# Optimization experiments

Measured on AMD Instinct MI355X. Metric: run time of the kernel, lower is better.

The kernel has to match this reference:

```python
import jax, jax.numpy as jnp
import numpy as np

N = 100000      # nodes
E = 1600000     # edges
F_IN = 256      # nfeat
F_OUT = 128     # out channels


def setup_inputs() -> dict:
    key = jax.random.key(0)
    k1, k2, k3 = jax.random.split(key, 3)
    feature = jax.random.normal(k1, (N, F_IN), dtype=jnp.float32)
    edge_index = jax.random.randint(k2, (2, E), 0, N, dtype=jnp.int32)
    # glorot-ish init for the GCN linear weight
    W = jax.random.normal(k3, (F_IN, F_OUT), dtype=jnp.float32) * (1.0 / np.sqrt(F_IN))
    b = jnp.zeros((F_OUT,), dtype=jnp.float32)
    return {"feature": feature, "edge_index": edge_index, "W": W, "b": b}


def reference(feature, edge_index, W, b):
    # GCNConv (PyG defaults): add self-loops, symmetric normalization,
    # linear transform then scatter-add aggregation to destination nodes.
    x = feature @ W                                   # [N, F_OUT]
    loops = jnp.arange(N, dtype=edge_index.dtype)
    row = jnp.concatenate([edge_index[0], loops])     # source nodes [E+N]
    col = jnp.concatenate([edge_index[1], loops])     # dest   nodes [E+N]
    ones = jnp.ones(row.shape[0], dtype=x.dtype)
    deg = jax.ops.segment_sum(ones, col, num_segments=N)   # in-degree incl. self-loop
    dinv = jnp.where(deg > 0, jax.lax.rsqrt(deg), 0.0)     # deg^{-1/2}
    norm = dinv[row] * dinv[col]                            # [E+N]
    msg = x[row] * norm[:, None]                            # gather + scale
    agg = jax.ops.segment_sum(msg, col, num_segments=N)     # scatter-add
    x_out = jax.nn.relu(agg + b)                            # [N, F_OUT]
    h = jax.nn.sigmoid(jnp.mean(x_out, axis=0))             # [F_OUT]
    return (x_out, h)
```

## Files before the change

### kernel.cpp

```cpp
#include <hip/hip_runtime.h>
#include <hip/hip_bf16.h>

typedef __attribute__((ext_vector_type(8))) short short8;
typedef __attribute__((ext_vector_type(4))) float floatx4;
typedef unsigned short u16;
typedef unsigned int u32;
typedef unsigned long long u64;

#define F_IN  256
#define F_OUT 128
#define CAP   64
#define NWIN  8
#define PRE   24

__device__ __forceinline__ float bf_lo(u32 u) { return __uint_as_float(u << 16); }
__device__ __forceinline__ float bf_hi(u32 u) { return __uint_as_float(u & 0xffff0000u); }
__device__ __forceinline__ u16 f2bf(float f) {
    u32 u = __float_as_uint(f);
    u += 0x7fffu + ((u >> 16) & 1u);
    return (u16)(u >> 16);
}

__global__ void k_pack(const float* __restrict__ W, u16* __restrict__ Wp,
                       u16* __restrict__ xw, int N) {
    int gid = blockIdx.x * 256 + threadIdx.x;
    if (gid < 32768) {
        int f = gid >> 3, j = gid & 7;
        int lane = f & 63, tt = (f >> 6) & 7, kb = f >> 9;
        int m = lane & 15, q = lane >> 4;
        Wp[(size_t)f * 8 + j] = f2bf(W[(kb * 32 + q * 8 + j) * F_OUT + tt * 16 + m]);
    } else {
        int e = gid - 32768;
        if (e < 128) {
            int w = e >> 4, m = e & 15;
            xw[((size_t)w * (N + 1) + N) * 16 + m] = 0;
        }
    }
}

__global__ void k_fillcap_xcd(const int* __restrict__ rowi, const int* __restrict__ coli,
                              int E, int npw, int N,
                              int* __restrict__ cursor, int* __restrict__ csr) {
    int grp  = blockIdx.x & (NWIN - 1);
    int gblk = blockIdx.x >> 3;
    int nblk = gridDim.x >> 3;
    int lo = grp * npw;
    int hi = lo + npw; if (hi > N) hi = N;
    for (int e = gblk * blockDim.x + threadIdx.x; e < E; e += nblk * blockDim.x) {
        int d = coli[e];
        if (d >= lo && d < hi) {
            int r = rowi[e];
            int p = atomicAdd(&cursor[d], 1);
            if (p < CAP) csr[((size_t)d << 6) + p] = r;
        }
    }
}

__global__ void k_degree(const int* __restrict__ col, int E, int* __restrict__ deg) {
    for (int e = blockIdx.x * blockDim.x + threadIdx.x; e < E; e += gridDim.x * blockDim.x)
        atomicAdd(&deg[col[e]], 1);
}

__global__ void k_blocksum(const int* __restrict__ deg, int N, int* __restrict__ bsum) {
    __shared__ int s[256];
    int base = blockIdx.x * 1024, t = threadIdx.x;
    int v = 0;
    for (int i = t; i < 1024; i += 256) { int idx = base + i; v += (idx < N) ? deg[idx] : 0; }
    s[t] = v; __syncthreads();
    for (int off = 128; off > 0; off >>= 1) {
        if (t < off) s[t] += s[t + off];
        __syncthreads();
    }
    if (t == 0) bsum[blockIdx.x] = s[0];
}

__global__ void k_rowptr(const int* __restrict__ deg, int N, const int* __restrict__ bsum,
                         int nb, int* __restrict__ rowptr) {
    __shared__ int s[256];
    __shared__ int sb[256];
    int base = blockIdx.x * 1024, t = threadIdx.x;
    sb[t] = (t < nb && t < blockIdx.x) ? bsum[t] : 0;
    __syncthreads();
    for (int off = 128; off > 0; off >>= 1) {
        if (t < off) sb[t] += sb[t + off];
        __syncthreads();
    }
    int blockbase = sb[0];
    int v[4]; int tot = 0;
#pragma unroll
    for (int j = 0; j < 4; ++j) {
        int idx = base + t * 4 + j;
        v[j] = (idx < N) ? deg[idx] : 0;
        tot += v[j];
    }
    s[t] = tot; __syncthreads();
    for (int off = 1; off < 256; off <<= 1) {
        int x = (t >= off) ? s[t - off] : 0;
        __syncthreads();
        s[t] += x;
        __syncthreads();
    }
    int prefix = blockbase + s[t] - tot;
#pragma unroll
    for (int j = 0; j < 4; ++j) {
        int idx = base + t * 4 + j;
        if (idx < N) rowptr[idx] = prefix;
        prefix += v[j];
    }
}

__global__ void k_fill(const int* __restrict__ rowi, const int* __restrict__ coli, int E,
                       const int* __restrict__ rowptr, int* __restrict__ cursor,
                       int* __restrict__ csr) {
    for (int e = blockIdx.x * blockDim.x + threadIdx.x; e < E; e += gridDim.x * blockDim.x) {
        int d = coli[e];
        int p = atomicAdd(&cursor[d], 1);
        csr[rowptr[d] + p] = rowi[e];
    }
}

__global__ __launch_bounds__(256) void k_gemm(
        const float* __restrict__ feat, const int* __restrict__ deg,
        const u16* __restrict__ Wp, u16* __restrict__ xw, int N) {
    __shared__ u16 atile[64 * 264];
    const int t = threadIdx.x, wave = t >> 6, lane = t & 63;
    const int m = lane & 15, q = lane >> 4;
    const int base = blockIdx.x * 64;

    for (int r = wave; r < 64; r += 4) {
        int i = base + r;
        float ax = 0.f, ay = 0.f, az = 0.f, aw = 0.f;
        if (i < N) {
            float di = rsqrtf((float)(deg[i] + 1));
            float4 v = *(const float4*)(feat + (size_t)i * F_IN + lane * 4);
            ax = di * v.x; ay = di * v.y; az = di * v.z; aw = di * v.w;
        }
        u32* dst = (u32*)(atile + r * 264 + lane * 4);
        dst[0] = ((u32)f2bf(ay) << 16) | (u32)f2bf(ax);
        dst[1] = ((u32)f2bf(aw) << 16) | (u32)f2bf(az);
    }
    __syncthreads();

    floatx4 acc[8];
#pragma unroll
    for (int tt = 0; tt < 8; ++tt) acc[tt] = (floatx4)0.0f;
    const short8* wp = (const short8*)Wp;
#pragma unroll
    for (int kb = 0; kb < 8; ++kb) {
        short8 a0 = *(const short8*)(atile + (wave * 16 + m) * 264 + kb * 32 + q * 8);
#pragma unroll
        for (int tt = 0; tt < 8; ++tt) {
            short8 b = wp[(kb * 8 + tt) * 64 + lane];
            acc[tt] = __builtin_amdgcn_mfma_f32_16x16x32_bf16(a0, b, acc[tt], 0, 0, 0);
        }
    }

#pragma unroll
    for (int r = 0; r < 4; ++r) {
        int orow = base + wave * 16 + q * 4 + r;
        if (orow < N) {
#pragma unroll
            for (int tt = 0; tt < 8; ++tt)
                xw[((size_t)tt * (N + 1) + orow) * 16 + m] = f2bf(acc[tt][r]);
        }
    }
}

__global__ __launch_bounds__(256) void k_agg(const u16* __restrict__ xw,
                                             const int* __restrict__ rowptr,
                                             const int* __restrict__ deg,
                                             const int* __restrict__ csr,
                                             const float* __restrict__ bvec,
                                             float* __restrict__ out,
                                             float* __restrict__ hsum, int N) {
    __shared__ float hpart[16];
    int t = threadIdx.x;
    if (t < 16) hpart[t] = 0.f;
    __syncthreads();
    const int w = blockIdx.x & 7;
    const int stripe = blockIdx.x >> 3;
    const int nstripe = gridDim.x >> 3;
    const int lane = t & 63, wv = t >> 6;
    const int lane3 = lane & 3;
    const int g = lane >> 2;
    const int gbase = lane & 60;
    const u32* slice = (const u32*)xw + (size_t)w * (N + 1) * 8;
    const float4 bv = *(const float4*)(bvec + w * 16 + lane3 * 4);
    float h0 = 0.f, h1 = 0.f, h2 = 0.f, h3 = 0.f;
    const int step = nstripe * 64;
    for (int i = stripe * 64 + wv * 16 + g; i < N; i += step) {
        int dd = deg[i];
        float di = rsqrtf((float)(dd + 1));
        int s0;
        if (rowptr) s0 = rowptr[i];
        else { s0 = i << 6; dd = dd < CAP ? dd : CAP; }
        u64 xs = *(const u64*)(slice + (u32)(i * 8) + lane3 * 2);
        u32 xsl = (u32)xs, xsh = (u32)(xs >> 32);
        float a0 = bf_lo(xsl), a1 = bf_hi(xsl), a2 = bf_lo(xsh), a3 = bf_hi(xsh);
        int s[6];
#pragma unroll
        for (int c = 0; c < 6; ++c) s[c] = csr[s0 + c * 4 + lane3];
#pragma unroll
        for (int c = 0; c < 6; ++c) s[c] = (c * 4 + lane3 < dd) ? s[c] : N;
        u64 xv[PRE];
#pragma unroll
        for (int u = 0; u < PRE; ++u) {
            int sx = __shfl(s[u >> 2], gbase + (u & 3));
            xv[u] = *(const u64*)(slice + (u32)(sx * 8) + lane3 * 2);
        }
#pragma unroll
        for (int u = 0; u < PRE; ++u) {
            u32 lo = (u32)xv[u], hi = (u32)(xv[u] >> 32);
            a0 += bf_lo(lo); a1 += bf_hi(lo); a2 += bf_lo(hi); a3 += bf_hi(hi);
        }
        if (__any(dd > PRE)) {
            int ddmax = dd;
            ddmax = max(ddmax, __shfl_xor(ddmax, 4));
            ddmax = max(ddmax, __shfl_xor(ddmax, 8));
            ddmax = max(ddmax, __shfl_xor(ddmax, 16));
            ddmax = max(ddmax, __shfl_xor(ddmax, 32));
            ddmax = min(ddmax, rowptr ? (1 << 20) : CAP);
            for (int jb = PRE; jb < ddmax; jb += 4) {
                int sxv = N;
                if (jb + lane3 < dd) sxv = csr[s0 + jb + lane3];
                u64 yv[4];
#pragma unroll
                for (int u = 0; u < 4; ++u) {
                    int sx = __shfl(sxv, gbase + u);
                    yv[u] = *(const u64*)(slice + (u32)(sx * 8) + lane3 * 2);
                }
#pragma unroll
                for (int u = 0; u < 4; ++u) {
                    u32 lo = (u32)yv[u], hi = (u32)(yv[u] >> 32);
                    a0 += bf_lo(lo); a1 += bf_hi(lo); a2 += bf_lo(hi); a3 += bf_hi(hi);
                }
            }
        }
        float o0 = fmaxf(fmaf(a0, di, bv.x), 0.f);
        float o1 = fmaxf(fmaf(a1, di, bv.y), 0.f);
        float o2 = fmaxf(fmaf(a2, di, bv.z), 0.f);
        float o3 = fmaxf(fmaf(a3, di, bv.w), 0.f);
        h0 += o0; h1 += o1; h2 += o2; h3 += o3;
        *(float4*)(out + (size_t)i * F_OUT + w * 16 + lane3 * 4) =
            make_float4(o0, o1, o2, o3);
    }
    atomicAdd(&hpart[lane3 * 4 + 0], h0);
    atomicAdd(&hpart[lane3 * 4 + 1], h1);
    atomicAdd(&hpart[lane3 * 4 + 2], h2);
    atomicAdd(&hpart[lane3 * 4 + 3], h3);
    __syncthreads();
    if (t < 16) atomicAdd(&hsum[w * 16 + t], hpart[t]);
}

__global__ void k_h(const float* __restrict__ hsum, float* __restrict__ outh, float invN) {
    int t = threadIdx.x;
    if (t < 128) {
        float mm = hsum[t] * invN;
        outh[t] = 1.f / (1.f + __expf(-mm));
    }
}

extern "C" void kernel_launch(void* const* d_in, const int* in_sizes, int n_in,
                              void* d_out, int out_size, void* d_ws, size_t ws_size,
                              hipStream_t stream) {
    const float* feat = (const float*)d_in[0];
    const int* ei     = (const int*)d_in[1];
    const float* W    = (const float*)d_in[2];
    const float* bvec = (const float*)d_in[3];
    float* out        = (float*)d_out;

    const int N = in_sizes[0] / F_IN;
    const int E = in_sizes[1] / 2;

    char* ws = (char*)d_ws;
    size_t o = 0;
    u16* Wp       = (u16*)(ws + o);   o += (size_t)F_IN * F_OUT * 2;
    int* deg      = (int*)(ws + o);   o += (size_t)N * 4;
    int* cursor   = (int*)(ws + o);   o += (size_t)N * 4;
    float* hsum   = (float*)(ws + o); o += 512;
    int* rowptr   = (int*)(ws + o);   o += (size_t)N * 4;
    int* bsum     = (int*)(ws + o);   o += 1024;
    size_t fixed  = o;

    size_t xw_bytes = (size_t)(N + 1) * F_OUT * 2;
    size_t need_fast = fixed + (size_t)N * CAP * 4 + xw_bytes;
    bool fast = ws_size >= need_fast + 4096;

    if (fast) {
        int* csr = (int*)(ws + o);    o += (size_t)N * CAP * 4;
        u16* xw  = (u16*)(ws + o);    o += xw_bytes;

        hipMemsetAsync((char*)cursor, 0, (size_t)N * 4 + 512, stream);
        k_pack<<<129, 256, 0, stream>>>(W, Wp, xw, N);
        int npw = (N + NWIN - 1) / NWIN;
        k_fillcap_xcd<<<2048, 256, 0, stream>>>(ei, ei + E, E, npw, N, cursor, csr);
        int ntiles = (N + 63) / 64;
        k_gemm<<<ntiles, 256, 0, stream>>>(feat, cursor, Wp, xw, N);
        k_agg<<<2048, 256, 0, stream>>>(xw, nullptr, cursor, csr, bvec, out, hsum, N);
        k_h<<<1, 128, 0, stream>>>(hsum, out + (size_t)N * F_OUT, 1.0f / (float)N);
    } else {
        int* csr = (int*)(ws + o);    o += (size_t)E * 4;
        u16* xw  = (u16*)(ws + o);    o += xw_bytes;

        hipMemsetAsync((char*)deg, 0, (size_t)N * 8 + 512, stream);
        k_pack<<<129, 256, 0, stream>>>(W, Wp, xw, N);
        k_degree<<<1024, 256, 0, stream>>>(ei + E, E, deg);
        int nb = (N + 1023) / 1024;
        k_blocksum<<<nb, 256, 0, stream>>>(deg, N, bsum);
        k_rowptr<<<nb, 256, 0, stream>>>(deg, N, bsum, nb, rowptr);
        k_fill<<<1024, 256, 0, stream>>>(ei, ei + E, E, rowptr, cursor, csr);
        int ntiles = (N + 63) / 64;
        k_gemm<<<ntiles, 256, 0, stream>>>(feat, deg, Wp, xw, N);
        k_agg<<<2048, 256, 0, stream>>>(xw, rowptr, deg, csr, bvec, out, hsum, N);
        k_h<<<1, 128, 0, stream>>>(hsum, out + (size_t)N * F_OUT, 1.0f / (float)N);
    }
}
```

Before: 366.9 us.

## Partition edges by destination window before scattering into capped CSR

Replaces the XCD-windowed fill kernel, which had every block group re-read the whole edge list and filter by destination range, with a two-pass partition. Each wave counts edges per window using ballots, reserves space with one atomic per window, and writes packed (dst,src) pairs into per-window buffers. A scatter kernel then reads only its window's edges to do the cursor atomics and CSR writes. This removes the eightfold re-reading of the edge list, at the cost of an extra workspace buffer, an extra kernel launch, and a write and read of 8-byte edge records.

```diff
diff --git a/kernel.cpp b/kernel.cpp
--- a/kernel.cpp
+++ b/kernel.cpp
@@ -35,6 +35,71 @@
             int w = e >> 4, m = e & 15;
             xw[((size_t)w * (N + 1) + N) * 16 + m] = 0;
         }
+    }
+}
+
+__global__ __launch_bounds__(256) void k_part(
+        const int* __restrict__ rowi, const int* __restrict__ coli, int E,
+        float npw_inv, int bcap, u64* __restrict__ ebuf, int* __restrict__ bcount) {
+    const int lane = threadIdx.x & 63;
+    const int wid = (blockIdx.x * blockDim.x + threadIdx.x) >> 6;
+    const int nwaves = (gridDim.x * blockDim.x) >> 6;
+    const int per = (E + nwaves - 1) / nwaves;
+    const int e0 = wid * per;
+    const int e1 = min(e0 + per, E);
+    if (e0 >= e1) return;
+    const u64 ltmask = (1ull << lane) - 1ull;
+
+    int cnt[NWIN];
+#pragma unroll
+    for (int wi = 0; wi < NWIN; ++wi) cnt[wi] = 0;
+    for (int cb = e0; cb < e1; cb += 64) {
+        int e = cb + lane;
+        int w = NWIN;
+        if (e < e1) w = (int)((float)coli[e] * npw_inv);
+#pragma unroll
+        for (int wi = 0; wi < NWIN; ++wi)
+            cnt[wi] += (int)__popcll(__ballot(w == wi));
+    }
+    int base[NWIN];
+#pragma unroll
+    for (int wi = 0; wi < NWIN; ++wi) {
+        int b = 0;
+        if (lane == 0 && cnt[wi] > 0) b = atomicAdd(&bcount[wi], cnt[wi]);
+        base[wi] = __shfl(b, 0);
+    }
+    for (int cb = e0; cb < e1; cb += 64) {
+        int e = cb + lane;
+        int w = NWIN, d = 0, r = 0;
+        if (e < e1) {
+            d = coli[e]; r = rowi[e];
+            w = (int)((float)d * npw_inv);
+        }
+        u64 v = ((u64)(u32)d << 32) | (u32)r;
+#pragma unroll
+        for (int wi = 0; wi < NWIN; ++wi) {
+            u64 mask = __ballot(w == wi);
+            if (w == wi) {
+                int off = base[wi] + (int)__popcll(mask & ltmask);
+                if (off < bcap) ebuf[(size_t)wi * bcap + off] = v;
+            }
+            base[wi] += (int)__popcll(mask);
+        }
+    }
+}
+
+__global__ __launch_bounds__(256) void k_scatter(
+        const u64* __restrict__ ebuf, const int* __restrict__ bcount, int bcap,
+        int* __restrict__ cursor, int* __restrict__ csr) {
+    int grp = blockIdx.x & (NWIN - 1);
+    int gblk = blockIdx.x >> 3, nblk = gridDim.x >> 3;
+    int n = min(bcount[grp], bcap);
+    const u64* buf = ebuf + (size_t)grp * bcap;
+    for (int k = gblk * blockDim.x + threadIdx.x; k < n; k += nblk * blockDim.x) {
+        u64 v = buf[k];
+        int d = (int)(v >> 32), r = (int)(u32)v;
+        int p = atomicAdd(&cursor[d], 1);
+        if (p < CAP) csr[((size_t)d << 6) + p] = r;
     }
 }
 
@@ -278,21 +343,38 @@
     int* deg      = (int*)(ws + o);   o += (size_t)N * 4;
     int* cursor   = (int*)(ws + o);   o += (size_t)N * 4;
     float* hsum   = (float*)(ws + o); o += 512;
+    int* bcount   = (int*)(ws + o);   o += 128;
     int* rowptr   = (int*)(ws + o);   o += (size_t)N * 4;
     int* bsum     = (int*)(ws + o);   o += 1024;
     size_t fixed  = o;
 
     size_t xw_bytes = (size_t)(N + 1) * F_OUT * 2;
-    size_t need_fast = fixed + (size_t)N * CAP * 4 + xw_bytes;
-    bool fast = ws_size >= need_fast + 4096;
-
-    if (fast) {
+    int bcap = E / NWIN + 32768;
+    size_t ebuf_bytes = (size_t)NWIN * bcap * 8;
+    size_t need_fast    = fixed + (size_t)N * CAP * 4 + xw_bytes;
+    size_t need_fastest = need_fast + ebuf_bytes;
+    int npw = (N + NWIN - 1) / NWIN;
+
+    if (ws_size >= need_fastest + 4096) {
         int* csr = (int*)(ws + o);    o += (size_t)N * CAP * 4;
         u16* xw  = (u16*)(ws + o);    o += xw_bytes;
-
-        hipMemsetAsync((char*)cursor, 0, (size_t)N * 4 + 512, stream);
+        u64* ebuf = (u64*)(ws + o);   o += ebuf_bytes;
+
+        hipMemsetAsync((char*)cursor, 0, (size_t)N * 4 + 640, stream);
         k_pack<<<129, 256, 0, stream>>>(W, Wp, xw, N);
-        int npw = (N + NWIN - 1) / NWIN;
+        k_part<<<1024, 256, 0, stream>>>(ei, ei + E, E, 1.0f / (float)npw,
+                                         bcap, ebuf, bcount);
+        k_scatter<<<2048, 256, 0, stream>>>(ebuf, bcount, bcap, cursor, csr);
+        int ntiles = (N + 63) / 64;
+        k_gemm<<<ntiles, 256, 0, stream>>>(feat, cursor, Wp, xw, N);
+        k_agg<<<2048, 256, 0, stream>>>(xw, nullptr, cursor, csr, bvec, out, hsum, N);
+        k_h<<<1, 128, 0, stream>>>(hsum, out + (size_t)N * F_OUT, 1.0f / (float)N);
+    } else if (ws_size >= need_fast + 4096) {
+        int* csr = (int*)(ws + o);    o += (size_t)N * CAP * 4;
+        u16* xw  = (u16*)(ws + o);    o += xw_bytes;
+
+        hipMemsetAsync((char*)cursor, 0, (size_t)N * 4 + 640, stream);
+        k_pack<<<129, 256, 0, stream>>>(W, Wp, xw, N);
         k_fillcap_xcd<<<2048, 256, 0, stream>>>(ei, ei + E, E, npw, N, cursor, csr);
         int ntiles = (N + 63) / 64;
         k_gemm<<<ntiles, 256, 0, stream>>>(feat, cursor, Wp, xw, N);
@@ -302,7 +384,7 @@
         int* csr = (int*)(ws + o);    o += (size_t)E * 4;
         u16* xw  = (u16*)(ws + o);    o += xw_bytes;
 
-        hipMemsetAsync((char*)deg, 0, (size_t)N * 8 + 512, stream);
+        hipMemsetAsync((char*)deg, 0, (size_t)N * 8 + 640, stream);
         k_pack<<<129, 256, 0, stream>>>(W, Wp, xw, N);
         k_degree<<<1024, 256, 0, stream>>>(ei + E, E, deg);
         int nb = (N + 1023) / 1024;
```

Result: slower. 749.1 us (+104.2%).
